# Optimization experiments

Measured on AMD Instinct MI355X. Metric: run time of the kernel, lower is better.

Reference implementation:

```python
import jax, jax.numpy as jnp
import numpy as np

B, S = 32, 128
VIN, VOUT = 32000, 32000
D, H, A = 256, 512, 128


def setup_inputs() -> dict:
    key = jax.random.key(0)
    ks = jax.random.split(key, 14)
    p = lambda k, sh: 0.02 * jax.random.normal(k, sh, jnp.float32)
    return {
        "tokens": jax.random.randint(ks[0], (B, S), 0, VIN + 1, dtype=jnp.int32),
        "emb": p(ks[1], (VIN + 1, D)),
        # forward encoder GRU (keras reset_after=True: separate input/recurrent bias)
        "Wx_f": p(ks[2], (D, 3 * H)), "Wh_f": p(ks[3], (H, 3 * H)),
        "bi_f": jnp.zeros((3 * H,), jnp.float32), "br_f": jnp.zeros((3 * H,), jnp.float32),
        # backward encoder GRU
        "Wx_b": p(ks[4], (D, 3 * H)), "Wh_b": p(ks[5], (H, 3 * H)),
        "bi_b": jnp.zeros((3 * H,), jnp.float32), "br_b": jnp.zeros((3 * H,), jnp.float32),
        # additive attention
        "W_a": p(ks[6], (A, H)), "U_a": p(ks[7], (A, 2 * H)), "V_a": p(ks[8], (1, A)),
        # decoder GRUCell (input = [enc_t, ctx] -> 4H)
        "Wx_d": p(ks[9], (4 * H, 3 * H)), "Wh_d": p(ks[10], (H, 3 * H)),
        "bi_d": jnp.zeros((3 * H,), jnp.float32), "br_d": jnp.zeros((3 * H,), jnp.float32),
        # output projection
        "Wo": p(ks[11], (H, VOUT + 1)), "bo": jnp.zeros((VOUT + 1,), jnp.float32),
    }


def _gru_step(h, x, Wx, Wh, bi, br):
    # keras GRU, gate order [z, r, h], reset_after=True
    gx = x @ Wx + bi
    gh = h @ Wh + br
    xz, xr, xh = jnp.split(gx, 3, axis=-1)
    hz, hr, hh = jnp.split(gh, 3, axis=-1)
    z = jax.nn.sigmoid(xz + hz)
    r = jax.nn.sigmoid(xr + hr)
    hc = jnp.tanh(xh + r * hh)
    return z * h + (1.0 - z) * hc


def _run_gru(xs, h0, Wx, Wh, bi, br):
    def f(h, x):
        hn = _gru_step(h, x, Wx, Wh, bi, br)
        return hn, hn
    return jax.lax.scan(f, h0, xs)  # xs: [S,B,D]


def _forward(tokens, emb, Wx_f, Wh_f, bi_f, br_f, Wx_b, Wh_b, bi_b, br_b,
             W_a, U_a, V_a, Wx_d, Wh_d, bi_d, br_d, Wo, bo):
    x = emb[tokens]                      # [B,S,D]
    xs = jnp.transpose(x, (1, 0, 2))     # [S,B,D]
    h0 = jnp.zeros((tokens.shape[0], H), x.dtype)
    _, ys_f = _run_gru(xs, h0, Wx_f, Wh_f, bi_f, br_f)
    hb, ys_b_rev = _run_gru(xs[::-1], h0, Wx_b, Wh_b, bi_b, br_b)
    enc_t = jnp.concatenate([ys_f, ys_b_rev[::-1]], axis=-1)  # [S,B,2H]
    enc = jnp.transpose(enc_t, (1, 0, 2))                     # [B,S,2H]
    U_enc = jnp.einsum('bsd,ad->bsa', enc, U_a)               # hoisted: loop-invariant
    v = V_a[0]                                                # [A]

    def dec_step(h, x_t):
        wh = h @ W_a.T                                        # [B,A]
        score = jnp.einsum('bsa,a->bs', jnp.tanh(wh[:, None, :] + U_enc), v)
        alpha = jax.nn.softmax(score, axis=-1)
        ctx = jnp.einsum('bs,bsd->bd', alpha, enc)            # [B,2H]
        din = jnp.concatenate([x_t, ctx], axis=-1)            # [B,4H]
        hn = _gru_step(h, din, Wx_d, Wh_d, bi_d, br_d)
        return hn, hn

    _, dec_seq = jax.lax.scan(dec_step, hb, enc_t)            # [S,B,H]
    dec = jnp.transpose(dec_seq, (1, 0, 2))                   # [B,S,H]
    logits = dec @ Wo + bo                                    # [B,S,VOUT+1]
    return jax.nn.softmax(logits, axis=-1)


def reference(tokens, emb, Wx_f, Wh_f, bi_f, br_f, Wx_b, Wh_b, bi_b, br_b,
              W_a, U_a, V_a, Wx_d, Wh_d, bi_d, br_d, Wo, bo):
    return _forward(tokens, emb, Wx_f, Wh_f, bi_f, br_f, Wx_b, Wh_b, bi_b, br_b,
                    W_a, U_a, V_a, Wx_d, Wh_d, bi_d, br_d, Wo, bo)
```

## Files before the change

### kernel.cpp

```cpp
#include <hip/hip_runtime.h>
#include <stdint.h>

typedef unsigned int u32;
typedef unsigned long long u64;
typedef __attribute__((ext_vector_type(8))) short bf16x8;
typedef __attribute__((ext_vector_type(4))) float f32x4;
typedef __attribute__((ext_vector_type(4))) int i32x4;
typedef __attribute__((ext_vector_type(2))) int i32x2;

#define DEV static __device__ __forceinline__

DEV short f2bf(float f){ u32 u=__float_as_uint(f); return (short)((u + 0x7fffu + ((u>>16)&1u))>>16); }
DEV float bf2f(short s){ return __uint_as_float(((u32)(unsigned short)s)<<16); }
DEV float sig_p(float x){ return 1.f/(1.f+expf(-x)); }
DEV float tanh_fast(float x){ float e=__expf(2.f*x); return 1.f-2.f/(e+1.f); }

DEV u32  cohl4(const u32* p){ return __hip_atomic_load(p, __ATOMIC_RELAXED, __HIP_MEMORY_SCOPE_AGENT); }
DEV void cohs4(u32* p, u32 v){ __hip_atomic_store(p, v, __ATOMIC_RELAXED, __HIP_MEMORY_SCOPE_AGENT); }
DEV u64  cohl8(const void* p){ return __hip_atomic_load((const u64*)p, __ATOMIC_RELAXED, __HIP_MEMORY_SCOPE_AGENT); }
DEV float cohlf(const float* p){ return __hip_atomic_load(p, __ATOMIC_RELAXED, __HIP_MEMORY_SCOPE_AGENT); }
DEV void cohsf(float* p, float v){ __hip_atomic_store(p, v, __ATOMIC_RELAXED, __HIP_MEMORY_SCOPE_AGENT); }
DEV void pollslot(const u32* s, u32 tgt){
  while (cohl4(s) < tgt) {}
}
DEV void filler_spin(const u32* done){
  float x = (float)threadIdx.x;
  while (cohl4(done) < 128u){
#pragma unroll
    for (int i=0;i<128;++i) x = __builtin_fmaf(x, 1.0000001f, 0.1f);
    asm volatile("" :: "v"(x));
  }
}


__global__ void cvt1d(const float* __restrict__ in, short* __restrict__ out, int n){
  int i = blockIdx.x*256 + threadIdx.x;
  if (i < n) out[i] = f2bf(in[i]);
}

__global__ void tconv(const float* __restrict__ in, short* __restrict__ out, int R, int C, int Cpad){
  __shared__ float t[32][33];
  int tx = threadIdx.x, ty = threadIdx.y;
  int c0 = blockIdx.x*32, r0 = blockIdx.y*32;
#pragma unroll
  for (int j=0;j<4;++j){
    int r = r0 + ty + 8*j, c = c0 + tx;
    t[ty+8*j][tx] = (c < C) ? in[(size_t)r*C + c] : 0.f;
  }
  __syncthreads();
#pragma unroll
  for (int j=0;j<4;++j){
    int oc = c0 + ty + 8*j;
    out[(size_t)oc*R + r0 + tx] = f2bf(t[tx][ty+8*j]);
  }
}

__global__ void btrans(const short* __restrict__ in, short* __restrict__ out, int Dd){
  __shared__ short t[32][33];
  int tx = threadIdx.x, ty = threadIdx.y;
  int d0 = blockIdx.x*32, s = blockIdx.y;
#pragma unroll
  for (int j=0;j<4;++j)
    t[ty+8*j][tx] = in[((size_t)s*Dd + d0 + ty + 8*j)*32 + tx];
  __syncthreads();
#pragma unroll
  for (int j=0;j<4;++j)
    out[((size_t)(s*32 + ty + 8*j))*Dd + d0 + tx] = t[tx][ty+8*j];
}

__global__ void etrans(const short* __restrict__ in, short* __restrict__ out){
  __shared__ short t[128][33];
  int c = blockIdx.x, tid = threadIdx.x;
#pragma unroll
  for (int i=0;i<16;++i){
    int idx = tid + i*256;
    t[idx>>5][idx&31] = in[((size_t)(idx>>5)*1536 + c)*32 + (idx&31)];
  }
  __syncthreads();
#pragma unroll
  for (int i=0;i<16;++i){
    int idx = tid + i*256;
    out[((size_t)(idx>>7)*1536 + c)*128 + (idx&127)] = t[idx&127][idx>>7];
  }
}

__global__ void embed_k(const int* __restrict__ tok, const float* __restrict__ emb, short* __restrict__ X){
  int row = blockIdx.x;
  int s = row >> 5, b = row & 31;
  int tv = tok[b*128 + s];
  X[(size_t)row*256 + threadIdx.x] = f2bf(emb[(size_t)tv*256 + threadIdx.x]);
}

template<int MODE>
__global__ __launch_bounds__(256) void gemm_k(
  const short* __restrict__ A, const short* __restrict__ BT,
  const float* __restrict__ bias, void* __restrict__ outp,
  float* __restrict__ psum, int Nreal, int K, int Ntot)
{
  const int m0 = blockIdx.y * 128, n0 = blockIdx.x * 128;
  const int tid = threadIdx.x, l = tid & 63, wv = tid >> 6;
  const int wm = wv >> 1, wn = wv & 1;
  __shared__ __align__(16) short As[128*64];
  __shared__ __align__(16) short Bs[128*64];
  f32x4 acc[4][4];
#pragma unroll
  for (int i=0;i<4;++i)
#pragma unroll
    for (int j=0;j<4;++j) acc[i][j] = (f32x4){0.f,0.f,0.f,0.f};

  const int nkb = K >> 6;
  for (int kb=0; kb<nkb; ++kb){
#pragma unroll
    for (int i=0;i<4;++i){
      int si = tid + i*256;
      int row = si >> 3, seg = si & 7;
      u32 off = (u32)(row*128 + seg*16) ^ (u32)((row&7)<<4);
      *(i32x4*)((char*)As + off) = *(const i32x4*)(A + (size_t)(m0+row)*K + kb*64 + seg*8);
      *(i32x4*)((char*)Bs + off) = *(const i32x4*)(BT + (size_t)(n0+row)*K + kb*64 + seg*8);
    }
    __syncthreads();
#pragma unroll
    for (int kt=0; kt<2; ++kt){
      bf16x8 af[4], bfv[4];
      int seg = kt*4 + (l>>4);
#pragma unroll
      for (int f=0; f<4; ++f){
        int ra = wm*64 + f*16 + (l&15);
        af[f]  = *(const bf16x8*)((char*)As + (((u32)(ra*128 + seg*16)) ^ ((u32)(ra&7)<<4)));
        int rb = wn*64 + f*16 + (l&15);
        bfv[f] = *(const bf16x8*)((char*)Bs + (((u32)(rb*128 + seg*16)) ^ ((u32)(rb&7)<<4)));
      }
#pragma unroll
      for (int mf=0; mf<4; ++mf)
#pragma unroll
        for (int nf=0; nf<4; ++nf)
          acc[mf][nf] = __builtin_amdgcn_mfma_f32_16x16x32_bf16(af[mf], bfv[nf], acc[mf][nf], 0,0,0);
    }
    __syncthreads();
  }

  if (MODE == 1){
    short* oT = (short*)outp;
#pragma unroll
    for (int mf=0; mf<4; ++mf){
      int r0 = m0 + wm*64 + mf*16 + ((l>>4)<<2);
      int s = r0 >> 5, b0 = r0 & 31;
#pragma unroll
      for (int nf=0; nf<4; ++nf){
        int col = n0 + wn*64 + nf*16 + (l&15);
        float bv = bias ? bias[col] : 0.f;
        short tmp[4];
#pragma unroll
        for (int j=0;j<4;++j) tmp[j] = f2bf(acc[mf][nf][j] + bv);
        *(i32x2*)(oT + ((size_t)s*Ntot + col)*32 + b0) = *(i32x2*)tmp;
      }
    }
  } else if (MODE == 3){
    short* o = (short*)outp;
#pragma unroll
    for (int mf=0; mf<4; ++mf){
      int r0 = m0 + wm*64 + mf*16 + ((l>>4)<<2);
#pragma unroll
      for (int nf=0; nf<4; ++nf){
        int col = n0 + wn*64 + nf*16 + (l&15);
        if (col < Nreal){
          float bv = bias ? bias[col] : 0.f;
#pragma unroll
          for (int j=0;j<4;++j) o[(size_t)(r0+j)*Nreal + col] = f2bf(acc[mf][nf][j] + bv);
        }
      }
    }
  } else {
    float* o = (float*)outp;
    int ncb = gridDim.x;
    float rs[4][4];
#pragma unroll
    for (int i=0;i<4;++i)
#pragma unroll
      for (int j=0;j<4;++j) rs[i][j]=0.f;
#pragma unroll
    for (int mf=0; mf<4; ++mf){
      int r0 = m0 + wm*64 + mf*16 + ((l>>4)<<2);
      int s = r0 >> 5, b0 = r0 & 31;
#pragma unroll
      for (int nf=0; nf<4; ++nf){
        int col = n0 + wn*64 + nf*16 + (l&15);
        if (col < Nreal){
          float bv = bias[col];
#pragma unroll
          for (int j=0;j<4;++j){
            float e = __expf(acc[mf][nf][j] + bv);
            o[(size_t)((b0+j)*128 + s)*Nreal + col] = e;
            rs[mf][j] += e;
          }
        }
      }
    }
#pragma unroll
    for (int mf=0; mf<4; ++mf)
#pragma unroll
      for (int j=0;j<4;++j){
        float v = rs[mf][j];
        v += __shfl_xor(v,1); v += __shfl_xor(v,2); v += __shfl_xor(v,4); v += __shfl_xor(v,8);
        if ((l&15)==0){
          int r = m0 + wm*64 + mf*16 + ((l>>4)<<2) + j;
          int orow = (r&31)*128 + (r>>5);
          psum[(size_t)orow*(2*ncb) + blockIdx.x*2 + wn] = v;
        }
      }
  }
}

__global__ __launch_bounds__(512,1) void enc_scan(
  const short* __restrict__ gxfT, const short* __restrict__ gxbT,
  const short* __restrict__ WhfT, const short* __restrict__ WhbT,
  const float* __restrict__ brf, const float* __restrict__ brb,
  float* __restrict__ hT, u32* __restrict__ hrowB,
  short* __restrict__ encT, u32* __restrict__ flags)
{
  const int tid = threadIdx.x, wg = blockIdx.x;
  if (wg >= 32){ filler_spin(&flags[0]); return; }

  __shared__ __align__(16) short As[32*512];
  __shared__ float accL[96][36];
  __shared__ float brL[96];
  const int dir = wg >> 4, j = wg & 15;
  const short* gxT = dir ? gxbT : gxfT;
  const short* WT  = dir ? WhbT : WhfT;
  const float* br  = dir ? brb  : brf;
  float* hTd  = hT + (size_t)dir*2*16384;
  u32* hrowBd = hrowB + (size_t)dir*2*8192;
  u32* flg    = flags + dir*16*32;
  const int l = tid & 63, wv = tid >> 6;

  if (tid < 96) brL[tid] = br[(tid>>5)*512 + j*32 + (tid&31)];

  bf16x8 bfr[2][16];
  if (wv < 3){
#pragma unroll
    for (int p=0;p<2;++p){
      int gcol = wv*512 + j*32 + p*16 + (l&15);
      const short* bp = WT + (size_t)gcol*512 + ((l>>4)<<3);
#pragma unroll
      for (int kt=0; kt<16; ++kt) bfr[p][kt] = *(const bf16x8*)(bp + kt*32);
    }
  }

  for (int t=0; t<128; ++t){
    const int s = dir ? (127-t) : t;
    const int cur = t & 1, nxt = cur ^ 1;
    if (t > 0){
      if (tid < 16) pollslot(&flg[tid*32], (u32)t);
      __syncthreads();
    }
#pragma unroll
    for (int it=0; it<8; ++it){
      int u = tid + it*512;
      int b = u >> 7, k4 = u & 127;
      u64 v = cohl8(&hrowBd[(cur*32 + b)*256 + k4*2]);
      *(u64*)((char*)As + b*1024 + ((k4*8) ^ ((b&15)<<4))) = v;
    }
    __syncthreads();
    if (wv < 3){
      f32x4 acc[2][2];
#pragma unroll
      for (int m=0;m<2;++m){ acc[m][0]=(f32x4){0,0,0,0}; acc[m][1]=(f32x4){0,0,0,0}; }
#pragma unroll
      for (int kt=0; kt<16; ++kt){
#pragma unroll
        for (int m=0;m<2;++m){
          int row = m*16 + (l&15);
          int kbyte = (kt*4 + (l>>4))*16;
          bf16x8 af = *(const bf16x8*)((char*)As + row*1024 + (kbyte ^ ((row&15)<<4)));
          acc[m][0] = __builtin_amdgcn_mfma_f32_16x16x32_bf16(af, bfr[0][kt], acc[m][0], 0,0,0);
          acc[m][1] = __builtin_amdgcn_mfma_f32_16x16x32_bf16(af, bfr[1][kt], acc[m][1], 0,0,0);
        }
      }
#pragma unroll
      for (int m=0;m<2;++m)
#pragma unroll
        for (int p=0;p<2;++p)
          *(f32x4*)&accL[wv*32 + p*16 + (l&15)][m*16 + ((l>>4)<<2)] = acc[m][p];
    }
    __syncthreads();
    {
      int b = tid & 31, hcp = tid >> 5;
      int hc0 = hcp*2;
      float hn[2];
#pragma unroll
      for (int q=0;q<2;++q){
        int hc = hc0 + q, hcol = j*32 + hc;
        float xz = bf2f(gxT[((size_t)s*1536 + hcol)*32 + b]);
        float xr = bf2f(gxT[((size_t)s*1536 + 512 + hcol)*32 + b]);
        float xh = bf2f(gxT[((size_t)s*1536 + 1024 + hcol)*32 + b]);
        float gz = accL[hc][b]    + brL[hc];
        float gr = accL[32+hc][b] + brL[32+hc];
        float gh = accL[64+hc][b] + brL[64+hc];
        float z = sig_p(xz + gz);
        float r = sig_p(xr + gr);
        float hcand = tanhf(xh + r*gh);
        float hp = hTd[cur*16384 + hcol*32 + b];
        hn[q] = z*hp + (1.f-z)*hcand;
        hTd[nxt*16384 + hcol*32 + b] = hn[q];
        encT[((size_t)s*1024 + dir*512 + hcol)*32 + b] = f2bf(hn[q]);
      }
      u32 pv = ((u32)(unsigned short)f2bf(hn[1])<<16) | (u32)(unsigned short)f2bf(hn[0]);
      cohs4(&hrowBd[(nxt*32 + b)*256 + j*16 + hcp], pv);
    }
    __syncthreads();
    if (tid == 0) cohs4(&flg[j*32], (u32)(t+1));
  }
}

__global__ void dec_init(const float* __restrict__ src, u32* __restrict__ hrowB){
  int i = blockIdx.x*256 + threadIdx.x;
  int b = i >> 8, k2 = i & 255;
  float v0 = src[(k2*2)*32 + b];
  float v1 = src[(k2*2+1)*32 + b];
  hrowB[b*256 + k2] = ((u32)(unsigned short)f2bf(v1)<<16) | (u32)(unsigned short)f2bf(v0);
}

__global__ __launch_bounds__(512,1) void dec_scan(
  const short* __restrict__ gxeR,
  const short* __restrict__ encx,
  const short* __restrict__ WhdT,
  const float* __restrict__ brd,
  const short* __restrict__ Wa, const short* __restrict__ Uenc, const float* __restrict__ Va,
  const float* __restrict__ h0,
  u32* __restrict__ hrowB,
  float* __restrict__ GH,
  short* __restrict__ decRow,
  u32* __restrict__ hflag, u32* __restrict__ gflag)
{
  const int tid = threadIdx.x, wg = blockIdx.x;
  if (wg >= 48){ filler_spin(&hflag[0]); return; }

  __shared__ __align__(16) short As[32*512];
  __shared__ float accL[96][36];
  __shared__ float hs[512];
  __shared__ float gxc[1536];
  __shared__ float brA[1536];
  __shared__ float whp[128*5];
  __shared__ float whv[128];
  __shared__ float scp[128*5];
  __shared__ float sc[128];
  __shared__ float red[4];
  __shared__ float vL[128];
  __shared__ float aL[128];

  const int l = tid & 63, wv = tid >> 6;

  if (wg < 16){
    const int j = wg;
    bf16x8 bfr[2][16];
    if (wv < 3){
#pragma unroll
      for (int p=0;p<2;++p){
        int gcol = wv*512 + j*32 + p*16 + (l&15);
        const short* bp = WhdT + (size_t)gcol*512 + ((l>>4)<<3);
#pragma unroll
        for (int kt=0; kt<16; ++kt) bfr[p][kt] = *(const bf16x8*)(bp + kt*32);
      }
    }
    for (int t=0; t<128; ++t){
      const int cur = t & 1;
      if (t > 0){
        if (tid < 32) pollslot(&hflag[tid*32], (u32)t);
        __syncthreads();
      }
#pragma unroll
      for (int it=0; it<8; ++it){
        int u = tid + it*512;
        int b = u >> 7, k4 = u & 127;
        u64 v = cohl8(&hrowB[((size_t)cur*32 + b)*256 + k4*2]);
        *(u64*)((char*)As + b*1024 + ((k4*8) ^ ((b&15)<<4))) = v;
      }
      __syncthreads();
      if (wv < 3){
        f32x4 acc[2][2];
#pragma unroll
        for (int m=0;m<2;++m){ acc[m][0]=(f32x4){0,0,0,0}; acc[m][1]=(f32x4){0,0,0,0}; }
#pragma unroll
        for (int kt=0; kt<16; ++kt){
#pragma unroll
          for (int m=0;m<2;++m){
            int row = m*16 + (l&15);
            int kbyte = (kt*4 + (l>>4))*16;
            bf16x8 af = *(const bf16x8*)((char*)As + row*1024 + (kbyte ^ ((row&15)<<4)));
            acc[m][0] = __builtin_amdgcn_mfma_f32_16x16x32_bf16(af, bfr[0][kt], acc[m][0], 0,0,0);
            acc[m][1] = __builtin_amdgcn_mfma_f32_16x16x32_bf16(af, bfr[1][kt], acc[m][1], 0,0,0);
          }
        }
#pragma unroll
        for (int m=0;m<2;++m)
#pragma unroll
          for (int p=0;p<2;++p)
            *(f32x4*)&accL[wv*32 + p*16 + (l&15)][m*16 + ((l>>4)<<2)] = acc[m][p];
      }
      __syncthreads();
#pragma unroll
      for (int i=0;i<6;++i){
        int idx = i*512 + tid;
        cohsf(&GH[(size_t)j*3072 + idx], accL[idx>>5][idx&31]);
      }
      __syncthreads();
      if (tid == 0) cohs4(&gflag[j*32], (u32)(t+1));
    }
  } else {
    const int b = wg - 16;
    u32 wa[64];
    {
      const u32* wp = (const u32*)(Wa + (size_t)(tid&127)*512 + (tid>>7)*128);
#pragma unroll
      for (int i=0;i<64;++i) wa[i] = wp[i];
    }
    u32 ue[16];
    {
      int s = tid & 127, aq = tid >> 7;
      const u32* up = (const u32*)(Uenc + ((size_t)(s*32 + b))*128 + aq*32);
#pragma unroll
      for (int i=0;i<16;++i) ue[i] = up[i];
    }
    if (tid < 128) vL[tid] = Va[tid];
    for (int i = tid; i < 1536; i += 512) brA[i] = brd[i];
    hs[tid] = h0[(size_t)tid*32 + b];
    const short* eb = encx + (size_t)b*1536*128;
    __syncthreads();

    for (int t=0; t<128; ++t){
      {
        int a = tid & 127, kq2 = tid >> 7;
        float p = 0.f;
        const float* hp2 = &hs[kq2*128];
#pragma unroll 8
        for (int i=0;i<64;++i){
          u32 w2 = wa[i];
          float2 h2 = *(const float2*)(hp2 + 2*i);
          p += bf2f((short)(w2 & 0xffff))*h2.x + bf2f((short)(w2 >> 16))*h2.y;
        }
        whp[a*5 + kq2] = p;
      }
      __syncthreads();
      if (tid < 128) whv[tid] = whp[tid*5]+whp[tid*5+1]+whp[tid*5+2]+whp[tid*5+3];
      __syncthreads();
      {
        int s = tid & 127, aq = tid >> 7;
        float p = 0.f;
#pragma unroll 4
        for (int i=0;i<16;++i){
          u32 u2 = ue[i];
          int a0 = aq*32 + 2*i;
          p += tanh_fast(whv[a0]   + bf2f((short)(u2 & 0xffff))) * vL[a0];
          p += tanh_fast(whv[a0+1] + bf2f((short)(u2 >> 16)))    * vL[a0+1];
        }
        scp[s*5 + aq] = p;
      }
      __syncthreads();
      if (tid < 128) sc[tid] = scp[tid*5]+scp[tid*5+1]+scp[tid*5+2]+scp[tid*5+3];
      __syncthreads();
      float ev = 0.f;
      if (tid < 128){
        float v = sc[tid], mx = v;
#pragma unroll
        for (int d2=32; d2; d2>>=1) mx = fmaxf(mx, __shfl_xor(mx, d2));
        if ((tid & 63) == 0) red[tid>>6] = mx;
      }
      __syncthreads();
      if (tid < 128){
        float mx = fmaxf(red[0], red[1]);
        ev = __expf(sc[tid] - mx);
        float sm = ev;
#pragma unroll
        for (int d2=32; d2; d2>>=1) sm += __shfl_xor(sm, d2);
        if ((tid & 63) == 0) red[2 + (tid>>6)] = sm;
      }
      __syncthreads();
      if (tid < 128) aL[tid] = ev / (red[2] + red[3]);
      __syncthreads();
      {
        int col = tid*3;
        float a0=0.f, a1=0.f, a2=0.f;
        const short* e0 = eb + (size_t)col*128;
#pragma unroll
        for (int sb=0; sb<16; ++sb){
          f32x4 av0 = *(const f32x4*)&aL[sb*8];
          f32x4 av1 = *(const f32x4*)&aL[sb*8+4];
          bf16x8 ev0 = *(const bf16x8*)(e0 + sb*8);
          bf16x8 ev1 = *(const bf16x8*)(e0 + 128 + sb*8);
          bf16x8 ev2 = *(const bf16x8*)(e0 + 256 + sb*8);
#pragma unroll
          for (int i=0;i<4;++i){
            a0 += bf2f(ev0[i])*av0[i]; a1 += bf2f(ev1[i])*av0[i]; a2 += bf2f(ev2[i])*av0[i];
            a0 += bf2f(ev0[4+i])*av1[i]; a1 += bf2f(ev1[4+i])*av1[i]; a2 += bf2f(ev2[4+i])*av1[i];
          }
        }
        gxc[col] = a0; gxc[col+1] = a1; gxc[col+2] = a2;
      }
      __syncthreads();
      const short* gx = gxeR + ((size_t)t*32 + b)*1536;
      float gx0 = bf2f(gx[tid])        + gxc[tid];
      float gx1 = bf2f(gx[512 + tid])  + gxc[512 + tid];
      float gx2 = bf2f(gx[1024 + tid]) + gxc[1024 + tid];
      if (tid < 16) pollslot(&gflag[tid*32], (u32)(t+1));
      __syncthreads();
      {
        size_t gb = (size_t)(tid>>5)*3072 + (size_t)(tid&31)*32 + b;
        float gh0 = cohlf(&GH[gb]);
        float gh1 = cohlf(&GH[gb + 1024]);
        float gh2 = cohlf(&GH[gb + 2048]);
        float z = sig_p(gx0 + gh0 + brA[tid]);
        float r = sig_p(gx1 + gh1 + brA[512 + tid]);
        float hcand = tanhf(gx2 + r*(gh2 + brA[1024 + tid]));
        float hp = hs[tid];
        float hn = z*hp + (1.f-z)*hcand;
        hs[tid] = hn;
        short mybf = f2bf(hn);
        decRow[((size_t)t*32 + b)*512 + tid] = mybf;
        u32 self16 = (u32)(unsigned short)mybf;
        u32 oth = (u32)__shfl_xor((int)self16, 1);
        if (!(tid & 1))
          cohs4(&hrowB[((size_t)((t+1)&1)*32 + b)*256 + (tid>>1)], self16 | (oth<<16));
      }
      __syncthreads();
      if (tid == 0) cohs4(&hflag[b*32], (u32)(t+1));
    }
  }
}

__global__ void scale_rows(float* __restrict__ out, const float* __restrict__ psum,
                           int ncols, int w){
  int r = blockIdx.x;
  __shared__ float ssum[256];
  float s = 0.f;
  for (int i = threadIdx.x; i < w; i += 256) s += psum[(size_t)r*w + i];
  ssum[threadIdx.x] = s; __syncthreads();
  for (int d = 128; d; d >>= 1){
    if (threadIdx.x < d) ssum[threadIdx.x] += ssum[threadIdx.x + d];
    __syncthreads();
  }
  float v = 1.f/ssum[0];
  float* p = out + (size_t)r*ncols;
  for (int i = threadIdx.x; i < ncols; i += 256) p[i] *= v;
}

extern "C" void kernel_launch(void* const* d_in, const int* in_sizes, int n_in,
                              void* d_out, int out_size, void* d_ws, size_t ws_size,
                              hipStream_t stream)
{
  const int*   tokens=(const int*)  d_in[0];
  const float* emb  =(const float*)d_in[1];
  const float* Wx_f =(const float*)d_in[2];
  const float* Wh_f =(const float*)d_in[3];
  const float* bi_f =(const float*)d_in[4];
  const float* br_f =(const float*)d_in[5];
  const float* Wx_b =(const float*)d_in[6];
  const float* Wh_b =(const float*)d_in[7];
  const float* bi_b =(const float*)d_in[8];
  const float* br_b =(const float*)d_in[9];
  const float* W_a  =(const float*)d_in[10];
  const float* U_a  =(const float*)d_in[11];
  const float* V_a  =(const float*)d_in[12];
  const float* Wx_d =(const float*)d_in[13];
  const float* Wh_d =(const float*)d_in[14];
  const float* bi_d =(const float*)d_in[15];
  const float* br_d =(const float*)d_in[16];
  const float* Wo   =(const float*)d_in[17];
  const float* bo   =(const float*)d_in[18];

  const int NV = 32001, NVP = 32128, NCB = 251;

  char* base = (char*)d_ws; size_t off = 0;
  auto alloc = [&](size_t bytes)->char*{
    off = (off + 255) & ~(size_t)255;
    char* p = base + off; off += bytes; return p;
  };
  u32*   flags  = (u32*)  alloc(16384);
  short* X      = (short*)alloc((size_t)4096*256*2);
  short* WxfT   = (short*)alloc((size_t)1536*256*2);
  short* WxbT   = (short*)alloc((size_t)1536*256*2);
  short* WhfT   = (short*)alloc((size_t)1536*512*2);
  short* WhbT   = (short*)alloc((size_t)1536*512*2);
  short* WhdT   = (short*)alloc((size_t)1536*512*2);
  short* WxeT   = (short*)alloc((size_t)1536*1024*2);
  short* WxcT   = (short*)alloc((size_t)1536*1024*2);
  short* WoT    = (short*)alloc((size_t)NVP*512*2);
  short* UaB    = (short*)alloc((size_t)128*1024*2);
  short* WaB    = (short*)alloc((size_t)128*512*2);
  short* gxfT   = (short*)alloc((size_t)128*1536*32*2);
  short* gxbT   = (short*)alloc((size_t)128*1536*32*2);
  short* encT   = (short*)alloc((size_t)128*1024*32*2);
  short* encRow = (short*)alloc((size_t)4096*1024*2);
  short* Uenc   = (short*)alloc((size_t)4096*128*2);
  short* gxeR   = (short*)alloc((size_t)4096*1536*2);
  short* encxT1 = (short*)alloc((size_t)128*1536*32*2);
  short* encx   = (short*)alloc((size_t)32*1536*128*2);
  short* decRow = (short*)alloc((size_t)4096*512*2);
  float* hT_e   = (float*)alloc((size_t)2*2*512*32*4);
  u32*   hrowB_e= (u32*)  alloc((size_t)2*2*32*256*4);
  u32*   hrowB_d= (u32*)  alloc((size_t)2*32*256*4);
  float* GH     = (float*)alloc((size_t)16*96*32*4);
  float* psum   = (float*)alloc((size_t)4096*2*NCB*4);

  hipMemsetAsync(flags, 0, 16384, stream);
  hipMemsetAsync(hT_e, 0, (size_t)2*2*512*32*4, stream);
  hipMemsetAsync(hrowB_e, 0, (size_t)2*2*32*256*4, stream);

  tconv<<<dim3(1536/32,256/32),dim3(32,8),0,stream>>>(Wx_f, WxfT, 256, 1536, 1536);
  tconv<<<dim3(1536/32,256/32),dim3(32,8),0,stream>>>(Wx_b, WxbT, 256, 1536, 1536);
  tconv<<<dim3(1536/32,512/32),dim3(32,8),0,stream>>>(Wh_f, WhfT, 512, 1536, 1536);
  tconv<<<dim3(1536/32,512/32),dim3(32,8),0,stream>>>(Wh_b, WhbT, 512, 1536, 1536);
  tconv<<<dim3(1536/32,512/32),dim3(32,8),0,stream>>>(Wh_d, WhdT, 512, 1536, 1536);
  tconv<<<dim3(1536/32,1024/32),dim3(32,8),0,stream>>>(Wx_d,                    WxeT, 1024, 1536, 1536);
  tconv<<<dim3(1536/32,1024/32),dim3(32,8),0,stream>>>(Wx_d+(size_t)1024*1536,  WxcT, 1024, 1536, 1536);
  tconv<<<dim3(NVP/32,512/32),dim3(32,8),0,stream>>>(Wo, WoT, 512, NV, NVP);
  cvt1d<<<(128*512+255)/256,256,0,stream>>>(W_a, WaB, 128*512);
  cvt1d<<<(128*1024+255)/256,256,0,stream>>>(U_a, UaB, 128*1024);

  embed_k<<<4096,256,0,stream>>>(tokens, emb, X);

  gemm_k<1><<<dim3(12,32),256,0,stream>>>(X, WxfT, bi_f, gxfT, nullptr, 1536, 256, 1536);
  gemm_k<1><<<dim3(12,32),256,0,stream>>>(X, WxbT, bi_b, gxbT, nullptr, 1536, 256, 1536);

  enc_scan<<<256,512,0,stream>>>(gxfT, gxbT, WhfT, WhbT, br_f, br_b,
                                 hT_e, hrowB_e, encT, flags);

  btrans<<<dim3(1024/32,128),dim3(32,8),0,stream>>>(encT, encRow, 1024);

  gemm_k<3><<<dim3(1,32),256,0,stream>>>(encRow, UaB, nullptr, Uenc, nullptr, 128, 1024, 128);
  gemm_k<3><<<dim3(12,32),256,0,stream>>>(encRow, WxeT, bi_d, gxeR, nullptr, 1536, 1024, 1536);
  gemm_k<1><<<dim3(12,32),256,0,stream>>>(encRow, WxcT, nullptr, encxT1, nullptr, 1536, 1024, 1536);
  etrans<<<1536,256,0,stream>>>(encxT1, encx);

  dec_init<<<32,256,0,stream>>>(hT_e + 32768, hrowB_d);

  dec_scan<<<256,512,0,stream>>>(gxeR, encx, WhdT, br_d, WaB, Uenc, V_a,
                                 hT_e + 32768, hrowB_d, GH, decRow,
                                 &flags[1024], &flags[2048]);

  gemm_k<2><<<dim3(NCB,32),256,0,stream>>>(decRow, WoT, bo, d_out, psum, NV, 512, NV);

  scale_rows<<<4096,256,0,stream>>>((float*)d_out, psum, NV, 2*NCB);
}
```

Baseline: 4.183 ms.

## Use per-timestep hidden-state bands and one-shot flags in persistent GRU scans

Replaces the double-buffered hidden-state exchange and counter flags with per-timestep buffers (hband/GHband) indexed by t, each with a write-once flag, so readers use plain 16-byte vector loads instead of coherent atomic 8-byte loads. The encoder keeps the previous hidden state in registers instead of reloading it from global memory, and the encT/decRow stores move after the flag signal so they leave the critical path. The filler-spin blocks that occupied the other CUs are removed, and the grids shrink to 32 and 48 blocks. The cost is larger scratch buffers and extra memsets. Plain loads of cross-block data also rely on stale cache lines never existing for fresh per-step addresses.

```diff
diff --git a/kernel.cpp b/kernel.cpp
--- a/kernel.cpp
+++ b/kernel.cpp
@@ -17,20 +17,8 @@
 
 DEV u32  cohl4(const u32* p){ return __hip_atomic_load(p, __ATOMIC_RELAXED, __HIP_MEMORY_SCOPE_AGENT); }
 DEV void cohs4(u32* p, u32 v){ __hip_atomic_store(p, v, __ATOMIC_RELAXED, __HIP_MEMORY_SCOPE_AGENT); }
-DEV u64  cohl8(const void* p){ return __hip_atomic_load((const u64*)p, __ATOMIC_RELAXED, __HIP_MEMORY_SCOPE_AGENT); }
-DEV float cohlf(const float* p){ return __hip_atomic_load(p, __ATOMIC_RELAXED, __HIP_MEMORY_SCOPE_AGENT); }
-DEV void cohsf(float* p, float v){ __hip_atomic_store(p, v, __ATOMIC_RELAXED, __HIP_MEMORY_SCOPE_AGENT); }
-DEV void pollslot(const u32* s, u32 tgt){
-  while (cohl4(s) < tgt) {}
-}
-DEV void filler_spin(const u32* done){
-  float x = (float)threadIdx.x;
-  while (cohl4(done) < 128u){
-#pragma unroll
-    for (int i=0;i<128;++i) x = __builtin_fmaf(x, 1.0000001f, 0.1f);
-    asm volatile("" :: "v"(x));
-  }
-}
+DEV void cohs8(void* p, u64 v){ __hip_atomic_store((u64*)p, v, __ATOMIC_RELAXED, __HIP_MEMORY_SCOPE_AGENT); }
+DEV void pollnz(const u32* s){ while (cohl4(s) == 0u) {} }
 
 
 __global__ void cvt1d(const float* __restrict__ in, short* __restrict__ out, int n){
@@ -215,22 +203,19 @@
   const short* __restrict__ gxfT, const short* __restrict__ gxbT,
   const short* __restrict__ WhfT, const short* __restrict__ WhbT,
   const float* __restrict__ brf, const float* __restrict__ brb,
-  float* __restrict__ hT, u32* __restrict__ hrowB,
-  short* __restrict__ encT, u32* __restrict__ flags)
+  u32* __restrict__ hband, float* __restrict__ hfin,
+  short* __restrict__ encT, u32* __restrict__ eflag)
 {
-  const int tid = threadIdx.x, wg = blockIdx.x;
-  if (wg >= 32){ filler_spin(&flags[0]); return; }
-
   __shared__ __align__(16) short As[32*512];
   __shared__ float accL[96][36];
   __shared__ float brL[96];
+  const int tid = threadIdx.x, wg = blockIdx.x;
   const int dir = wg >> 4, j = wg & 15;
   const short* gxT = dir ? gxbT : gxfT;
   const short* WT  = dir ? WhbT : WhfT;
   const float* br  = dir ? brb  : brf;
-  float* hTd  = hT + (size_t)dir*2*16384;
-  u32* hrowBd = hrowB + (size_t)dir*2*8192;
-  u32* flg    = flags + dir*16*32;
+  u32* hb = hband + (size_t)dir*129*8192;
+  u32* fl = eflag + (size_t)dir*129*512;
   const int l = tid & 63, wv = tid >> 6;
 
   if (tid < 96) brL[tid] = br[(tid>>5)*512 + j*32 + (tid&31)];
@@ -246,19 +231,21 @@
     }
   }
 
+  const int pb = tid & 31, php = tid >> 5;
+  float hreg[2] = {0.f, 0.f};
+
   for (int t=0; t<128; ++t){
     const int s = dir ? (127-t) : t;
-    const int cur = t & 1, nxt = cur ^ 1;
     if (t > 0){
-      if (tid < 16) pollslot(&flg[tid*32], (u32)t);
-      __syncthreads();
-    }
-#pragma unroll
-    for (int it=0; it<8; ++it){
+      if (tid < 16) pollnz(&fl[(size_t)t*512 + tid*32]);
+      __syncthreads();
+    }
+#pragma unroll
+    for (int it=0; it<4; ++it){
       int u = tid + it*512;
-      int b = u >> 7, k4 = u & 127;
-      u64 v = cohl8(&hrowBd[(cur*32 + b)*256 + k4*2]);
-      *(u64*)((char*)As + b*1024 + ((k4*8) ^ ((b&15)<<4))) = v;
+      int b = u >> 6, k8 = u & 63;
+      i32x4 v = *(const i32x4*)&hb[(size_t)t*8192 + b*256 + k8*4];
+      *(i32x4*)((char*)As + b*1024 + ((k8*16) ^ ((b&15)<<4))) = v;
     }
     __syncthreads();
     if (wv < 3){
@@ -283,10 +270,9 @@
           *(f32x4*)&accL[wv*32 + p*16 + (l&15)][m*16 + ((l>>4)<<2)] = acc[m][p];
     }
     __syncthreads();
+    short obf[2];
     {
-      int b = tid & 31, hcp = tid >> 5;
-      int hc0 = hcp*2;
-      float hn[2];
+      int b = pb, hc0 = php*2;
 #pragma unroll
       for (int q=0;q<2;++q){
         int hc = hc0 + q, hcol = j*32 + hc;
@@ -299,25 +285,33 @@
         float z = sig_p(xz + gz);
         float r = sig_p(xr + gr);
         float hcand = tanhf(xh + r*gh);
-        float hp = hTd[cur*16384 + hcol*32 + b];
-        hn[q] = z*hp + (1.f-z)*hcand;
-        hTd[nxt*16384 + hcol*32 + b] = hn[q];
-        encT[((size_t)s*1024 + dir*512 + hcol)*32 + b] = f2bf(hn[q]);
-      }
-      u32 pv = ((u32)(unsigned short)f2bf(hn[1])<<16) | (u32)(unsigned short)f2bf(hn[0]);
-      cohs4(&hrowBd[(nxt*32 + b)*256 + j*16 + hcp], pv);
+        float hn = z*hreg[q] + (1.f-z)*hcand;
+        hreg[q] = hn;
+        obf[q] = f2bf(hn);
+      }
+      u32 pv = ((u32)(unsigned short)obf[1]<<16) | (u32)(unsigned short)obf[0];
+      cohs4(&hb[(size_t)(t+1)*8192 + b*256 + j*16 + php], pv);
     }
     __syncthreads();
-    if (tid == 0) cohs4(&flg[j*32], (u32)(t+1));
-  }
-}
-
-__global__ void dec_init(const float* __restrict__ src, u32* __restrict__ hrowB){
+    if (tid == 0) cohs4(&fl[(size_t)(t+1)*512 + j*32], 1u);
+    {
+      int b = pb, hc0 = php*2;
+      encT[((size_t)s*1024 + dir*512 + (j*32+hc0))*32 + b]   = obf[0];
+      encT[((size_t)s*1024 + dir*512 + (j*32+hc0+1))*32 + b] = obf[1];
+      if (dir && t == 127){
+        hfin[(j*32+hc0)*32 + b]   = hreg[0];
+        hfin[(j*32+hc0+1)*32 + b] = hreg[1];
+      }
+    }
+  }
+}
+
+__global__ void dec_init(const float* __restrict__ hfin, u32* __restrict__ hband0){
   int i = blockIdx.x*256 + threadIdx.x;
   int b = i >> 8, k2 = i & 255;
-  float v0 = src[(k2*2)*32 + b];
-  float v1 = src[(k2*2+1)*32 + b];
-  hrowB[b*256 + k2] = ((u32)(unsigned short)f2bf(v1)<<16) | (u32)(unsigned short)f2bf(v0);
+  float v0 = hfin[(k2*2)*32 + b];
+  float v1 = hfin[(k2*2+1)*32 + b];
+  hband0[b*256 + k2] = ((u32)(unsigned short)f2bf(v1)<<16) | (u32)(unsigned short)f2bf(v0);
 }
 
 __global__ __launch_bounds__(512,1) void dec_scan(
@@ -326,15 +320,12 @@
   const short* __restrict__ WhdT,
   const float* __restrict__ brd,
   const short* __restrict__ Wa, const short* __restrict__ Uenc, const float* __restrict__ Va,
-  const float* __restrict__ h0,
-  u32* __restrict__ hrowB,
-  float* __restrict__ GH,
+  const float* __restrict__ hfin,
+  u32* __restrict__ hband,
+  float* __restrict__ GHband,
   short* __restrict__ decRow,
   u32* __restrict__ hflag, u32* __restrict__ gflag)
 {
-  const int tid = threadIdx.x, wg = blockIdx.x;
-  if (wg >= 48){ filler_spin(&hflag[0]); return; }
-
   __shared__ __align__(16) short As[32*512];
   __shared__ float accL[96][36];
   __shared__ float hs[512];
@@ -348,6 +339,7 @@
   __shared__ float vL[128];
   __shared__ float aL[128];
 
+  const int tid = threadIdx.x, wg = blockIdx.x;
   const int l = tid & 63, wv = tid >> 6;
 
   if (wg < 16){
@@ -362,18 +354,18 @@
         for (int kt=0; kt<16; ++kt) bfr[p][kt] = *(const bf16x8*)(bp + kt*32);
       }
     }
+    const int b2 = tid >> 4, q = tid & 15;
     for (int t=0; t<128; ++t){
-      const int cur = t & 1;
       if (t > 0){
-        if (tid < 32) pollslot(&hflag[tid*32], (u32)t);
+        if (tid < 32) pollnz(&hflag[(size_t)t*1024 + tid*32]);
         __syncthreads();
       }
 #pragma unroll
-      for (int it=0; it<8; ++it){
+      for (int it=0; it<4; ++it){
         int u = tid + it*512;
-        int b = u >> 7, k4 = u & 127;
-        u64 v = cohl8(&hrowB[((size_t)cur*32 + b)*256 + k4*2]);
-        *(u64*)((char*)As + b*1024 + ((k4*8) ^ ((b&15)<<4))) = v;
+        int b = u >> 6, k8 = u & 63;
+        i32x4 v = *(const i32x4*)&hband[(size_t)t*8192 + b*256 + k8*4];
+        *(i32x4*)((char*)As + b*1024 + ((k8*16) ^ ((b&15)<<4))) = v;
       }
       __syncthreads();
       if (wv < 3){
@@ -398,13 +390,18 @@
             *(f32x4*)&accL[wv*32 + p*16 + (l&15)][m*16 + ((l>>4)<<2)] = acc[m][p];
       }
       __syncthreads();
-#pragma unroll
-      for (int i=0;i<6;++i){
-        int idx = i*512 + tid;
-        cohsf(&GH[(size_t)j*3072 + idx], accL[idx>>5][idx&31]);
-      }
-      __syncthreads();
-      if (tid == 0) cohs4(&gflag[j*32], (u32)(t+1));
+      {
+        float* gbase = GHband + ((size_t)t*32 + b2)*1536;
+#pragma unroll
+        for (int pp=0; pp<3; ++pp){
+          int cp = q*6 + pp*2;
+          float f0 = accL[cp][b2], f1 = accL[cp+1][b2];
+          u64 pv = ((u64)__float_as_uint(f1)<<32) | (u64)__float_as_uint(f0);
+          cohs8(&gbase[(cp>>5)*512 + j*32 + (cp&31)], pv);
+        }
+      }
+      __syncthreads();
+      if (tid == 0) cohs4(&gflag[(size_t)t*512 + j*32], 1u);
     }
   } else {
     const int b = wg - 16;
@@ -423,7 +420,7 @@
     }
     if (tid < 128) vL[tid] = Va[tid];
     for (int i = tid; i < 1536; i += 512) brA[i] = brd[i];
-    hs[tid] = h0[(size_t)tid*32 + b];
+    hs[tid] = hfin[(size_t)tid*32 + b];
     const short* eb = encx + (size_t)b*1536*128;
     __syncthreads();
 
@@ -501,28 +498,29 @@
       float gx0 = bf2f(gx[tid])        + gxc[tid];
       float gx1 = bf2f(gx[512 + tid])  + gxc[512 + tid];
       float gx2 = bf2f(gx[1024 + tid]) + gxc[1024 + tid];
-      if (tid < 16) pollslot(&gflag[tid*32], (u32)(t+1));
-      __syncthreads();
+      if (tid < 16) pollnz(&gflag[(size_t)t*512 + tid*32]);
+      __syncthreads();
+      short mybf;
       {
-        size_t gb = (size_t)(tid>>5)*3072 + (size_t)(tid&31)*32 + b;
-        float gh0 = cohlf(&GH[gb]);
-        float gh1 = cohlf(&GH[gb + 1024]);
-        float gh2 = cohlf(&GH[gb + 2048]);
+        const float* ghp = GHband + ((size_t)t*32 + b)*1536;
+        float gh0 = ghp[tid];
+        float gh1 = ghp[512 + tid];
+        float gh2 = ghp[1024 + tid];
         float z = sig_p(gx0 + gh0 + brA[tid]);
         float r = sig_p(gx1 + gh1 + brA[512 + tid]);
         float hcand = tanhf(gx2 + r*(gh2 + brA[1024 + tid]));
         float hp = hs[tid];
         float hn = z*hp + (1.f-z)*hcand;
         hs[tid] = hn;
-        short mybf = f2bf(hn);
-        decRow[((size_t)t*32 + b)*512 + tid] = mybf;
+        mybf = f2bf(hn);
         u32 self16 = (u32)(unsigned short)mybf;
         u32 oth = (u32)__shfl_xor((int)self16, 1);
         if (!(tid & 1))
-          cohs4(&hrowB[((size_t)((t+1)&1)*32 + b)*256 + (tid>>1)], self16 | (oth<<16));
-      }
-      __syncthreads();
-      if (tid == 0) cohs4(&hflag[b*32], (u32)(t+1));
+          cohs4(&hband[(size_t)(t+1)*8192 + b*256 + (tid>>1)], self16 | (oth<<16));
+      }
+      __syncthreads();
+      if (tid == 0) cohs4(&hflag[(size_t)(t+1)*1024 + b*32], 1u);
+      decRow[((size_t)t*32 + b)*512 + tid] = mybf;
     }
   }
 }
@@ -574,7 +572,13 @@
     off = (off + 255) & ~(size_t)255;
     char* p = base + off; off += bytes; return p;
   };
-  u32*   flags  = (u32*)  alloc(16384);
+  u32*   eflag  = (u32*)  alloc((size_t)2*129*512*4);
+  u32*   hflag  = (u32*)  alloc((size_t)129*1024*4);
+  u32*   gflag  = (u32*)  alloc((size_t)128*512*4);
+  u32*   hband_e= (u32*)  alloc((size_t)2*129*8192*4);
+  u32*   hband_d= (u32*)  alloc((size_t)129*8192*4);
+  float* GHband = (float*)alloc((size_t)128*32*1536*4);
+  float* hfin   = (float*)alloc((size_t)512*32*4);
   short* X      = (short*)alloc((size_t)4096*256*2);
   short* WxfT   = (short*)alloc((size_t)1536*256*2);
   short* WxbT   = (short*)alloc((size_t)1536*256*2);
@@ -595,15 +599,12 @@
   short* encxT1 = (short*)alloc((size_t)128*1536*32*2);
   short* encx   = (short*)alloc((size_t)32*1536*128*2);
   short* decRow = (short*)alloc((size_t)4096*512*2);
-  float* hT_e   = (float*)alloc((size_t)2*2*512*32*4);
-  u32*   hrowB_e= (u32*)  alloc((size_t)2*2*32*256*4);
-  u32*   hrowB_d= (u32*)  alloc((size_t)2*32*256*4);
-  float* GH     = (float*)alloc((size_t)16*96*32*4);
   float* psum   = (float*)alloc((size_t)4096*2*NCB*4);
 
-  hipMemsetAsync(flags, 0, 16384, stream);
-  hipMemsetAsync(hT_e, 0, (size_t)2*2*512*32*4, stream);
-  hipMemsetAsync(hrowB_e, 0, (size_t)2*2*32*256*4, stream);
+  hipMemsetAsync(eflag, 0, (size_t)2*129*512*4, stream);
+  hipMemsetAsync(hflag, 0, (size_t)129*1024*4, stream);
+  hipMemsetAsync(gflag, 0, (size_t)128*512*4, stream);
+  hipMemsetAsync(hband_e, 0, (size_t)2*129*8192*4, stream);
 
   tconv<<<dim3(1536/32,256/32),dim3(32,8),0,stream>>>(Wx_f, WxfT, 256, 1536, 1536);
   tconv<<<dim3(1536/32,256/32),dim3(32,8),0,stream>>>(Wx_b, WxbT, 256, 1536, 1536);
@@ -621,8 +622,8 @@
   gemm_k<1><<<dim3(12,32),256,0,stream>>>(X, WxfT, bi_f, gxfT, nullptr, 1536, 256, 1536);
   gemm_k<1><<<dim3(12,32),256,0,stream>>>(X, WxbT, bi_b, gxbT, nullptr, 1536, 256, 1536);
 
-  enc_scan<<<256,512,0,stream>>>(gxfT, gxbT, WhfT, WhbT, br_f, br_b,
-                                 hT_e, hrowB_e, encT, flags);
+  enc_scan<<<32,512,0,stream>>>(gxfT, gxbT, WhfT, WhbT, br_f, br_b,
+                                hband_e, hfin, encT, eflag);
 
   btrans<<<dim3(1024/32,128),dim3(32,8),0,stream>>>(encT, encRow, 1024);
 
@@ -631,11 +632,10 @@
   gemm_k<1><<<dim3(12,32),256,0,stream>>>(encRow, WxcT, nullptr, encxT1, nullptr, 1536, 1024, 1536);
   etrans<<<1536,256,0,stream>>>(encxT1, encx);
 
-  dec_init<<<32,256,0,stream>>>(hT_e + 32768, hrowB_d);
-
-  dec_scan<<<256,512,0,stream>>>(gxeR, encx, WhdT, br_d, WaB, Uenc, V_a,
-                                 hT_e + 32768, hrowB_d, GH, decRow,
-                                 &flags[1024], &flags[2048]);
+  dec_init<<<32,256,0,stream>>>(hfin, hband_d);
+
+  dec_scan<<<48,512,0,stream>>>(gxeR, encx, WhdT, br_d, WaB, Uenc, V_a,
+                                hfin, hband_d, GHband, decRow, hflag, gflag);
 
   gemm_k<2><<<dim3(NCB,32),256,0,stream>>>(decRow, WoT, bo, d_out, psum, NV, 512, NV);
 
```

Measured after the change: 3.783 ms. 9.6% less time.
